# Kernel optimization log

Measured on AMD Instinct MI355X. Metric: run time of the kernel, lower is better.

The kernel has to match this reference:

```python
import jax, jax.numpy as jnp
import numpy as np

N_NODES = 50000
N_GRAPHS = 64
HIDDEN = 128
INPUT = 128
NEG_SLOPE = 0.2


def _gat_layer(x, src, dst, W, a_src, a_dst, b, n_nodes):
    # x: [N, Fin]; src/dst: [E] (self-loops already included)
    h = x @ W                              # [N, H]
    alpha_s = h @ a_src                    # [N]
    alpha_d = h @ a_dst                    # [N]
    e = alpha_s[src] + alpha_d[dst]        # [E]
    e = jnp.where(e > 0, e, NEG_SLOPE * e)  # leaky_relu(0.2)
    # segment softmax over destination node
    m = jax.ops.segment_max(e, dst, num_segments=n_nodes)  # [N]
    m = jnp.where(jnp.isfinite(m), m, 0.0)
    ee = jnp.exp(e - m[dst])
    s = jax.ops.segment_sum(ee, dst, num_segments=n_nodes)
    coef = ee / (s[dst] + 1e-16)           # [E]
    out = jax.ops.segment_sum(h[src] * coef[:, None], dst, num_segments=n_nodes)
    return out + b


def setup_inputs() -> dict:
    key = jax.random.key(0)
    ks = jax.random.split(key, 16)
    x = jax.random.normal(ks[0], (N_NODES, INPUT), dtype=jnp.float32)
    edge_index = jax.random.randint(ks[1], (2, 600000), 0, N_NODES, dtype=jnp.int64 if jax.config.x64_enabled else jnp.int32).astype(jnp.int32)
    batch = jnp.sort(jax.random.randint(ks[2], (N_NODES,), 0, N_GRAPHS)).astype(jnp.int32)
    def glorot(k, shape):
        lim = float(np.sqrt(6.0 / (shape[0] + shape[-1])))
        return jax.random.uniform(k, shape, jnp.float32, -lim, lim)
    params = {}
    dims = [(INPUT, HIDDEN), (HIDDEN, HIDDEN), (HIDDEN, HIDDEN)]
    for i, (fi, fo) in enumerate(dims, 1):
        params[f"W{i}"] = glorot(ks[3 * i], (fi, fo))
        params[f"a_src{i}"] = glorot(ks[3 * i + 1], (fo,)) * 0.1
        params[f"a_dst{i}"] = glorot(ks[3 * i + 2], (fo,)) * 0.1
        params[f"b{i}"] = jnp.zeros((fo,), jnp.float32)
    return dict(x=x, edge_index=edge_index, batch=batch, **params)


def reference(x, edge_index, batch,
              W1, a_src1, a_dst1, b1,
              W2, a_src2, a_dst2, b2,
              W3, a_src3, a_dst3, b3):
    n = x.shape[0]
    loops = jnp.arange(n, dtype=edge_index.dtype)
    src = jnp.concatenate([edge_index[0], loops])  # PyG add_self_loops=True
    dst = jnp.concatenate([edge_index[1], loops])
    h = jax.nn.elu(_gat_layer(x, src, dst, W1, a_src1, a_dst1, b1, n))
    h = jax.nn.elu(_gat_layer(h, src, dst, W2, a_src2, a_dst2, b2, n))
    h = jax.nn.elu(_gat_layer(h, src, dst, W3, a_src3, a_dst3, b3, n))
    # global_mean_pool
    sums = jax.ops.segment_sum(h, batch, num_segments=N_GRAPHS)
    cnt = jax.ops.segment_sum(jnp.ones((n,), h.dtype), batch, num_segments=N_GRAPHS)
    return sums / jnp.maximum(cnt, 1.0)[:, None]
```

## Files before the change

kernel.cpp:

```cpp
#include <hip/hip_runtime.h>
#include <math.h>

#define N_NODES 50000
#define N_GRAPHS 64
#define HID 128
#define SCAN_B 196

typedef _Float16 half8 __attribute__((ext_vector_type(8)));
typedef float f32x4 __attribute__((ext_vector_type(4)));
typedef int i32x4 __attribute__((ext_vector_type(4)));

__device__ __forceinline__ float lrelu(float e) { return e > 0.f ? e : 0.2f * e; }
__device__ __forceinline__ float elu_fast(float o) { return o > 0.f ? o : __expf(o) - 1.f; }

__device__ __forceinline__ void fmix_lo(float& a, int h2, float c) {
    asm("v_fma_mix_f32 %0, %1, %2, %0 op_sel_hi:[1,0,0]" : "+v"(a) : "v"(h2), "v"(c));
}
__device__ __forceinline__ void fmix_hi(float& a, int h2, float c) {
    asm("v_fma_mix_f32 %0, %1, %2, %0 op_sel:[1,0,0] op_sel_hi:[1,0,0]" : "+v"(a) : "v"(h2), "v"(c));
}

__global__ void count_prep(const int* __restrict__ dst, int n_e, int nblk,
                           int* __restrict__ counts, int* __restrict__ start,
                           const float* __restrict__ W0, const float* __restrict__ W1,
                           const float* __restrict__ W2,
                           const float* __restrict__ as0, const float* __restrict__ ad0,
                           const float* __restrict__ as1, const float* __restrict__ ad1,
                           const float* __restrict__ as2, const float* __restrict__ ad2,
                           _Float16* __restrict__ Wh0, _Float16* __restrict__ Wh1,
                           _Float16* __restrict__ Wh2,
                           float* __restrict__ wfold) {
    int blk = blockIdx.x;
    if (blk < nblk) {
        if (blk == 0 && threadIdx.x <= N_GRAPHS) start[threadIdx.x] = -1;
        int e = blk * 256 + threadIdx.x;
        if (e < n_e) atomicAdd(&counts[dst[e]], 1);
        return;
    }
    int b = blk - nblk;
    if (b < 24) {
        int layer = b >> 3;
        const float* W = layer == 0 ? W0 : (layer == 1 ? W1 : W2);
        _Float16* Wh = layer == 0 ? Wh0 : (layer == 1 ? Wh1 : Wh2);
        int t = (b & 7) * 256 + threadIdx.x;
        int lane = t & 63;
        int nt = (t >> 6) & 7;
        int kt = t >> 9;
        int n = nt * 16 + (lane & 15);
        int kbase = kt * 32 + (lane >> 4) * 8;
#pragma unroll
        for (int j = 0; j < 8; ++j) {
            float w = W[(size_t)(kbase + j) * 128 + n];
            Wh[(size_t)t * 8 + j] = (_Float16)w;
        }
    } else {
        int idx = b - 24;
        int layer = idx >> 1, which = idx & 1;
        const float* W = layer == 0 ? W0 : (layer == 1 ? W1 : W2);
        const float* a = which == 0 ? (layer == 0 ? as0 : (layer == 1 ? as1 : as2))
                                    : (layer == 0 ? ad0 : (layer == 1 ? ad1 : ad2));
        int k = threadIdx.x;
        if (k < 128) {
            float s = 0.f;
            for (int j = 0; j < 128; ++j) s = fmaf(W[k * 128 + j], a[j], s);
            wfold[idx * 128 + k] = s;
        }
    }
}

__global__ __launch_bounds__(256) void block_reduce(const int* __restrict__ counts,
                                                    int* __restrict__ bsum) {
    __shared__ int red[256];
    int t = threadIdx.x;
    int i = blockIdx.x * 256 + t;
    red[t] = (i < N_NODES) ? counts[i] : 0;
    __syncthreads();
#pragma unroll
    for (int off = 128; off; off >>= 1) {
        if (t < off) red[t] += red[t + off];
        __syncthreads();
    }
    if (t == 0) bsum[blockIdx.x] = red[0];
}

__global__ __launch_bounds__(256) void block_scan(const int* __restrict__ counts,
                                                  const int* __restrict__ bsum,
                                                  const int* __restrict__ batch,
                                                  int* __restrict__ offs,
                                                  int* __restrict__ cursor,
                                                  int* __restrict__ start) {
    __shared__ int sb[256];
    __shared__ int sh[256];
    int t = threadIdx.x;
    int v = (t < SCAN_B) ? bsum[t] : 0;
    sb[t] = v;
    __syncthreads();
#pragma unroll
    for (int off = 1; off < 256; off <<= 1) {
        int u = (t >= off) ? sb[t - off] : 0;
        __syncthreads();
        sb[t] += u;
        __syncthreads();
    }
    int bpre = (blockIdx.x == 0) ? 0 : sb[blockIdx.x - 1];
    if (blockIdx.x == 0 && t == SCAN_B - 1) offs[N_NODES] = sb[t];

    int i = blockIdx.x * 256 + t;
    int c = (i < N_NODES) ? counts[i] : 0;
    sh[t] = c;
    __syncthreads();
#pragma unroll
    for (int off = 1; off < 256; off <<= 1) {
        int u = (t >= off) ? sh[t - off] : 0;
        __syncthreads();
        sh[t] += u;
        __syncthreads();
    }
    if (i < N_NODES) {
        int e = bpre + sh[t] - c;
        offs[i] = e;
        cursor[i] = e;
        int b = batch[i];
        if (i == 0) start[b] = 0;
        else if (batch[i - 1] != b) start[b] = i;
    }
}

__global__ void scatter_kernel(const int* __restrict__ src, const int* __restrict__ dst, int n_e,
                               int* __restrict__ cursor, int* __restrict__ csr_src,
                               float* __restrict__ outz) {
    int gid = blockIdx.x * blockDim.x + threadIdx.x;
    if (gid < N_GRAPHS * HID) outz[gid] = 0.f;
    if (gid >= n_e) return;
    int d = dst[gid];
    int pos = atomicAdd(&cursor[d], 1);
    csr_src[pos] = src[gid];
}

__global__ __launch_bounds__(256) void gemm_mfma(const float* __restrict__ X,
                                                 const _Float16* __restrict__ Wh,
                                                 const float* __restrict__ wsv,
                                                 const float* __restrict__ wdv,
                                                 _Float16* __restrict__ H16,
                                                 float* __restrict__ AS,
                                                 float* __restrict__ AD) {
    __shared__ float wsL[128], wdL[128];
    int t = threadIdx.x;
    if (t < 128) wsL[t] = wsv[t];
    else if (t < 256) wdL[t - 128] = wdv[t - 128];
    __syncthreads();

    int wave = t >> 6, lane = t & 63;
    int m15 = lane & 15, quad = lane >> 4;
    int rowbase = blockIdx.x * 64 + wave * 16;
    int arow = rowbase + m15;
    bool arow_ok = arow < N_NODES;

    f32x4 acc[8];
#pragma unroll
    for (int nt = 0; nt < 8; ++nt) acc[nt] = (f32x4){0.f, 0.f, 0.f, 0.f};
    float as_p = 0.f, ad_p = 0.f;

    const float* xrow = X + (size_t)arow * 128 + quad * 8;
#pragma unroll
    for (int kt = 0; kt < 4; ++kt) {
        f32x4 a0 = (f32x4){0.f, 0.f, 0.f, 0.f};
        f32x4 a1 = (f32x4){0.f, 0.f, 0.f, 0.f};
        if (arow_ok) {
            a0 = *(const f32x4*)(xrow + kt * 32);
            a1 = *(const f32x4*)(xrow + kt * 32 + 4);
        }
        int kb = kt * 32 + quad * 8;
        half8 ah;
#pragma unroll
        for (int j = 0; j < 4; ++j) {
            as_p = fmaf(a0[j], wsL[kb + j], as_p);
            ad_p = fmaf(a0[j], wdL[kb + j], ad_p);
            as_p = fmaf(a1[j], wsL[kb + 4 + j], as_p);
            ad_p = fmaf(a1[j], wdL[kb + 4 + j], ad_p);
            ah[j] = (_Float16)a0[j];
            ah[4 + j] = (_Float16)a1[j];
        }
#pragma unroll
        for (int nt = 0; nt < 8; ++nt) {
            size_t fidx = ((size_t)((kt * 8 + nt) * 64 + lane)) * 8;
            half8 bh = *(const half8*)(Wh + fidx);
            acc[nt] = __builtin_amdgcn_mfma_f32_16x16x32_f16(ah, bh, acc[nt], 0, 0, 0);
        }
    }

#pragma unroll
    for (int nt = 0; nt < 8; ++nt) {
        int c = nt * 16 + m15;
#pragma unroll
        for (int reg = 0; reg < 4; ++reg) {
            int gr = rowbase + quad * 4 + reg;
            if (gr < N_NODES) H16[(size_t)gr * 128 + c] = (_Float16)acc[nt][reg];
        }
    }
    as_p += __shfl_xor(as_p, 16);
    ad_p += __shfl_xor(ad_p, 16);
    as_p += __shfl_xor(as_p, 32);
    ad_p += __shfl_xor(ad_p, 32);
    if (quad == 0 && arow_ok) { AS[arow] = as_p; AD[arow] = ad_p; }
}

__global__ __launch_bounds__(256) void aggregate_kernel(const _Float16* __restrict__ H16,
                                                        const float* __restrict__ AS,
                                                        const float* __restrict__ AD,
                                                        const int* __restrict__ offs,
                                                        const int* __restrict__ csr_src,
                                                        const float* __restrict__ bias,
                                                        float* __restrict__ OUT) {
    __shared__ int2 sh_sp[16][64];
    int tid = threadIdx.x;
    int quad = tid >> 4;
    int l16 = tid & 15;
    int node = blockIdx.x * 16 + quad;

    int beg = offs[node];
    int deg = offs[node + 1] - beg;
    float ad = AD[node];
    float eself = lrelu(AS[node] + ad);
    bool fast = deg <= 64;

    float m, inv, psn;
    if (fast) {
        float mym = -INFINITY;
        for (int i = l16; i < deg; i += 16) {
            int sv = csr_src[beg + i];
            float e = lrelu(AS[sv] + ad);
            sh_sp[quad][i] = make_int2(sv, __float_as_int(e));
            mym = fmaxf(mym, e);
        }
#pragma unroll
        for (int off = 8; off; off >>= 1) mym = fmaxf(mym, __shfl_xor(mym, off, 16));
        m = fmaxf(mym, eself);
        float ssum = 0.f;
        for (int i = l16; i < deg; i += 16) {
            int2 sp = sh_sp[quad][i];
            float p = __expf(__int_as_float(sp.y) - m);
            sh_sp[quad][i] = make_int2(sp.x, __float_as_int(p));
            ssum += p;
        }
#pragma unroll
        for (int off = 8; off; off >>= 1) ssum += __shfl_xor(ssum, off, 16);
        float ps = __expf(eself - m);
        inv = __builtin_amdgcn_rcpf(ssum + ps + 1e-16f);
        psn = ps * inv;
    } else {
        float mym = -INFINITY;
        for (int i = beg + l16; i < beg + deg; i += 16)
            mym = fmaxf(mym, lrelu(AS[csr_src[i]] + ad));
#pragma unroll
        for (int off = 8; off; off >>= 1) mym = fmaxf(mym, __shfl_xor(mym, off, 16));
        m = fmaxf(mym, eself);
        float ssum = 0.f;
        for (int i = beg + l16; i < beg + deg; i += 16)
            ssum += __expf(lrelu(AS[csr_src[i]] + ad) - m);
#pragma unroll
        for (int off = 8; off; off >>= 1) ssum += __shfl_xor(ssum, off, 16);
        float ps = __expf(eself - m);
        inv = __builtin_amdgcn_rcpf(ssum + ps + 1e-16f);
        psn = ps * inv;
    }

    const i32x4* H4 = (const i32x4*)H16;
    float accA[8] = {0.f, 0.f, 0.f, 0.f, 0.f, 0.f, 0.f, 0.f};
    float accB[8] = {0.f, 0.f, 0.f, 0.f, 0.f, 0.f, 0.f, 0.f};

    if (fast) {
        int k = 0;
        for (; k + 1 < deg; k += 2) {
            int2 sp0 = sh_sp[quad][k];
            int2 sp1 = sh_sp[quad][k + 1];
            float c0 = __int_as_float(sp0.y) * inv;
            float c1 = __int_as_float(sp1.y) * inv;
            i32x4 h0 = H4[(size_t)sp0.x * 16 + l16];
            i32x4 h1 = H4[(size_t)sp1.x * 16 + l16];
#pragma unroll
            for (int j = 0; j < 4; ++j) {
                fmix_lo(accA[2 * j], h0[j], c0);
                fmix_hi(accA[2 * j + 1], h0[j], c0);
                fmix_lo(accB[2 * j], h1[j], c1);
                fmix_hi(accB[2 * j + 1], h1[j], c1);
            }
        }
        if (k < deg) {
            int2 sp0 = sh_sp[quad][k];
            float c0 = __int_as_float(sp0.y) * inv;
            i32x4 h0 = H4[(size_t)sp0.x * 16 + l16];
#pragma unroll
            for (int j = 0; j < 4; ++j) {
                fmix_lo(accA[2 * j], h0[j], c0);
                fmix_hi(accA[2 * j + 1], h0[j], c0);
            }
        }
    } else {
        for (int k = 0; k < deg; ++k) {
            int s = csr_src[beg + k];
            float c = __expf(lrelu(AS[s] + ad) - m) * inv;
            i32x4 h0 = H4[(size_t)s * 16 + l16];
#pragma unroll
            for (int j = 0; j < 4; ++j) {
                fmix_lo(accA[2 * j], h0[j], c);
                fmix_hi(accA[2 * j + 1], h0[j], c);
            }
        }
    }

    i32x4 hsv = H4[(size_t)node * 16 + l16];
#pragma unroll
    for (int j = 0; j < 4; ++j) {
        fmix_lo(accA[2 * j], hsv[j], psn);
        fmix_hi(accA[2 * j + 1], hsv[j], psn);
    }
    f32x4 b0 = ((const f32x4*)bias)[l16 * 2];
    f32x4 b1 = ((const f32x4*)bias)[l16 * 2 + 1];
    f32x4 o0, o1;
    o0.x = elu_fast(accA[0] + accB[0] + b0.x);
    o0.y = elu_fast(accA[1] + accB[1] + b0.y);
    o0.z = elu_fast(accA[2] + accB[2] + b0.z);
    o0.w = elu_fast(accA[3] + accB[3] + b0.w);
    o1.x = elu_fast(accA[4] + accB[4] + b1.x);
    o1.y = elu_fast(accA[5] + accB[5] + b1.y);
    o1.z = elu_fast(accA[6] + accB[6] + b1.z);
    o1.w = elu_fast(accA[7] + accB[7] + b1.w);
    ((f32x4*)OUT)[(size_t)node * 32 + l16 * 2] = o0;
    ((f32x4*)OUT)[(size_t)node * 32 + l16 * 2 + 1] = o1;
}

__device__ __forceinline__ int estart(const int* __restrict__ start, int g) {
    for (; g < N_GRAPHS; ++g) {
        int v = start[g];
        if (v >= 0) return v;
    }
    return N_NODES;
}

__global__ __launch_bounds__(128) void pool_kernel(const float* __restrict__ F,
                                                   const int* __restrict__ start,
                                                   float* __restrict__ out) {
    int b = blockIdx.x;
    int g = b >> 4, sub = b & 15;
    int c = threadIdx.x;
    int s0 = estart(start, g), e0 = estart(start, g + 1);
    float acc = 0.f;
    for (int i = s0 + sub; i < e0; i += 16) acc += F[(size_t)i * 128 + c];
    int cnt = e0 - s0;
    float r = 1.f / (float)(cnt > 1 ? cnt : 1);
    atomicAdd(&out[(size_t)g * 128 + c], acc * r);
}

extern "C" void kernel_launch(void* const* d_in, const int* in_sizes, int n_in,
                              void* d_out, int out_size, void* d_ws, size_t ws_size,
                              hipStream_t stream) {
    const float* x = (const float*)d_in[0];
    const int* edge_index = (const int*)d_in[1];
    const int* batch = (const int*)d_in[2];
    const float* W[3]   = {(const float*)d_in[3], (const float*)d_in[7], (const float*)d_in[11]};
    const float* avs[3] = {(const float*)d_in[4], (const float*)d_in[8], (const float*)d_in[12]};
    const float* avd[3] = {(const float*)d_in[5], (const float*)d_in[9], (const float*)d_in[13]};
    const float* bb[3]  = {(const float*)d_in[6], (const float*)d_in[10], (const float*)d_in[14]};
    int E0 = in_sizes[1] / 2;
    const int* esrc = edge_index;
    const int* edst = edge_index + E0;

    char* p = (char*)d_ws;
    auto alloc = [&](size_t bytes) -> void* {
        void* q = (void*)p;
        p += (bytes + 255) & ~(size_t)255;
        return q;
    };
    int* counts   = (int*)alloc((size_t)N_NODES * 4);
    int* offs     = (int*)alloc((size_t)(N_NODES + 1) * 4);
    int* cursor   = (int*)alloc((size_t)N_NODES * 4);
    int* csr_src  = (int*)alloc((size_t)E0 * 4);
    int* start    = (int*)alloc((N_GRAPHS + 1) * 4);
    int* bsum     = (int*)alloc(SCAN_B * 4);
    float* AS     = (float*)alloc((size_t)N_NODES * 4);
    float* AD     = (float*)alloc((size_t)N_NODES * 4);
    float* wfold  = (float*)alloc(6 * 128 * 4);
    _Float16* H16 = (_Float16*)alloc((size_t)N_NODES * HID * 2);
    float* FA     = (float*)alloc((size_t)N_NODES * HID * 4);
    float* FB     = (float*)alloc((size_t)N_NODES * HID * 4);
    _Float16* Wh[3];
    for (int l = 0; l < 3; ++l) Wh[l] = (_Float16*)alloc(16384 * 2);

    int nblk = (E0 + 255) / 256;
    hipMemsetAsync(counts, 0, (size_t)N_NODES * 4, stream);
    count_prep<<<nblk + 30, 256, 0, stream>>>(edst, E0, nblk, counts, start,
                                              W[0], W[1], W[2], avs[0], avd[0], avs[1], avd[1],
                                              avs[2], avd[2], Wh[0], Wh[1], Wh[2], wfold);
    block_reduce<<<SCAN_B, 256, 0, stream>>>(counts, bsum);
    block_scan<<<SCAN_B, 256, 0, stream>>>(counts, bsum, batch, offs, cursor, start);
    scatter_kernel<<<nblk, 256, 0, stream>>>(esrc, edst, E0, cursor, csr_src, (float*)d_out);

    const float* cur = x;
    float* feat[2] = {FA, FB};
    for (int l = 0; l < 3; ++l) {
        gemm_mfma<<<(N_NODES + 63) / 64, 256, 0, stream>>>(cur, Wh[l],
                                                           wfold + (l * 2) * 128,
                                                           wfold + (l * 2 + 1) * 128,
                                                           H16, AS, AD);
        float* nxt = feat[l & 1];
        aggregate_kernel<<<N_NODES / 16, 256, 0, stream>>>(H16, AS, AD, offs, csr_src,
                                                           bb[l], nxt);
        cur = nxt;
    }

    pool_kernel<<<N_GRAPHS * 16, 128, 0, stream>>>(cur, start, (float*)d_out);
}
```

Before: 304.2 us.

## Sort nodes by degree for aggregation and defer softmax normalization

Builds a degree histogram during the scan and a degree-bucketed node ordering during the scatter pass. The aggregate kernel then processes nodes in that order, so the 16 nodes sharing a block have similar degree and their 16-lane groups finish at similar times. Softmax normalization is deferred to the final output (multiply by the reciprocal once), the self-row load is hoisted, and the gather loop is unrolled by 4 for more loads in flight. Costs include an extra indirection, atomics for the ordering, and scattered output writes and offs reads because node order is no longer sequential.

```diff
diff --git a/kernel.cpp b/kernel.cpp
--- a/kernel.cpp
+++ b/kernel.cpp
@@ -5,6 +5,8 @@
 #define N_GRAPHS 64
 #define HID 128
 #define SCAN_B 196
+#define NODE_BLKS 196
+#define NBUCK 128
 
 typedef _Float16 half8 __attribute__((ext_vector_type(8)));
 typedef float f32x4 __attribute__((ext_vector_type(4)));
@@ -22,6 +24,7 @@
 
 __global__ void count_prep(const int* __restrict__ dst, int n_e, int nblk,
                            int* __restrict__ counts, int* __restrict__ start,
+                           int* __restrict__ dhist, int* __restrict__ gcur,
                            const float* __restrict__ W0, const float* __restrict__ W1,
                            const float* __restrict__ W2,
                            const float* __restrict__ as0, const float* __restrict__ ad0,
@@ -32,7 +35,10 @@
                            float* __restrict__ wfold) {
     int blk = blockIdx.x;
     if (blk < nblk) {
-        if (blk == 0 && threadIdx.x <= N_GRAPHS) start[threadIdx.x] = -1;
+        if (blk == 0) {
+            if (threadIdx.x <= N_GRAPHS) start[threadIdx.x] = -1;
+            if (threadIdx.x < NBUCK) { dhist[threadIdx.x] = 0; gcur[threadIdx.x] = 0; }
+        }
         int e = blk * 256 + threadIdx.x;
         if (e < n_e) atomicAdd(&counts[dst[e]], 1);
         return;
@@ -88,10 +94,13 @@
                                                   const int* __restrict__ batch,
                                                   int* __restrict__ offs,
                                                   int* __restrict__ cursor,
-                                                  int* __restrict__ start) {
+                                                  int* __restrict__ start,
+                                                  int* __restrict__ dhist) {
     __shared__ int sb[256];
     __shared__ int sh[256];
+    __shared__ int lh[NBUCK];
     int t = threadIdx.x;
+    if (t < NBUCK) lh[t] = 0;
     int v = (t < SCAN_B) ? bsum[t] : 0;
     sb[t] = v;
     __syncthreads();
@@ -123,18 +132,60 @@
         int b = batch[i];
         if (i == 0) start[b] = 0;
         else if (batch[i - 1] != b) start[b] = i;
-    }
-}
-
-__global__ void scatter_kernel(const int* __restrict__ src, const int* __restrict__ dst, int n_e,
-                               int* __restrict__ cursor, int* __restrict__ csr_src,
-                               float* __restrict__ outz) {
-    int gid = blockIdx.x * blockDim.x + threadIdx.x;
+        atomicAdd(&lh[c < NBUCK - 1 ? c : NBUCK - 1], 1);
+    }
+    __syncthreads();
+    if (t < NBUCK) {
+        int n = lh[t];
+        if (n) atomicAdd(&dhist[t], n);
+    }
+}
+
+__global__ __launch_bounds__(256) void scatter_kernel(const int* __restrict__ src,
+                                                      const int* __restrict__ dst, int n_e,
+                                                      int* __restrict__ cursor,
+                                                      int* __restrict__ csr_src,
+                                                      float* __restrict__ outz,
+                                                      const int* __restrict__ offs,
+                                                      const int* __restrict__ dhist,
+                                                      int* __restrict__ gcur,
+                                                      int* __restrict__ order) {
+    int gid = blockIdx.x * 256 + threadIdx.x;
     if (gid < N_GRAPHS * HID) outz[gid] = 0.f;
-    if (gid >= n_e) return;
-    int d = dst[gid];
-    int pos = atomicAdd(&cursor[d], 1);
-    csr_src[pos] = src[gid];
+    if (gid < n_e) {
+        int d = dst[gid];
+        int pos = atomicAdd(&cursor[d], 1);
+        csr_src[pos] = src[gid];
+    }
+    if (blockIdx.x >= NODE_BLKS) return;
+
+    __shared__ int lh[NBUCK], sc[NBUCK], lbase[NBUCK];
+    int t = threadIdx.x;
+    if (t < NBUCK) lh[t] = 0;
+    __syncthreads();
+    int b = -1, lpos = 0;
+    if (gid < N_NODES) {
+        int deg = offs[gid + 1] - offs[gid];
+        b = deg < NBUCK - 1 ? deg : NBUCK - 1;
+        lpos = atomicAdd(&lh[b], 1);
+    }
+    __syncthreads();
+    if (t < NBUCK) sc[t] = dhist[t];
+    __syncthreads();
+    for (int off = 1; off < NBUCK; off <<= 1) {
+        int u = (t < NBUCK && t >= off) ? sc[t - off] : 0;
+        __syncthreads();
+        if (t < NBUCK) sc[t] += u;
+        __syncthreads();
+    }
+    if (t < NBUCK) {
+        int excl = t ? sc[t - 1] : 0;
+        int cnt = lh[t];
+        int bb = cnt ? atomicAdd(&gcur[t], cnt) : 0;
+        lbase[t] = excl + bb;
+    }
+    __syncthreads();
+    if (gid < N_NODES) order[lbase[b] + lpos] = gid;
 }
 
 __global__ __launch_bounds__(256) void gemm_mfma(const float* __restrict__ X,
@@ -210,21 +261,24 @@
                                                         const float* __restrict__ AD,
                                                         const int* __restrict__ offs,
                                                         const int* __restrict__ csr_src,
+                                                        const int* __restrict__ order,
                                                         const float* __restrict__ bias,
                                                         float* __restrict__ OUT) {
     __shared__ int2 sh_sp[16][64];
     int tid = threadIdx.x;
     int quad = tid >> 4;
     int l16 = tid & 15;
-    int node = blockIdx.x * 16 + quad;
+    int node = order[blockIdx.x * 16 + quad];
 
     int beg = offs[node];
     int deg = offs[node + 1] - beg;
     float ad = AD[node];
     float eself = lrelu(AS[node] + ad);
+    const i32x4* H4 = (const i32x4*)H16;
+    i32x4 hsv = H4[(size_t)node * 16 + l16];
     bool fast = deg <= 64;
 
-    float m, inv, psn;
+    float m, ssum = 0.f, ps;
     if (fast) {
         float mym = -INFINITY;
         for (int i = l16; i < deg; i += 16) {
@@ -236,18 +290,13 @@
 #pragma unroll
         for (int off = 8; off; off >>= 1) mym = fmaxf(mym, __shfl_xor(mym, off, 16));
         m = fmaxf(mym, eself);
-        float ssum = 0.f;
+        ps = __expf(eself - m);
         for (int i = l16; i < deg; i += 16) {
             int2 sp = sh_sp[quad][i];
             float p = __expf(__int_as_float(sp.y) - m);
             sh_sp[quad][i] = make_int2(sp.x, __float_as_int(p));
             ssum += p;
         }
-#pragma unroll
-        for (int off = 8; off; off >>= 1) ssum += __shfl_xor(ssum, off, 16);
-        float ps = __expf(eself - m);
-        inv = __builtin_amdgcn_rcpf(ssum + ps + 1e-16f);
-        psn = ps * inv;
     } else {
         float mym = -INFINITY;
         for (int i = beg + l16; i < beg + deg; i += 16)
@@ -255,29 +304,27 @@
 #pragma unroll
         for (int off = 8; off; off >>= 1) mym = fmaxf(mym, __shfl_xor(mym, off, 16));
         m = fmaxf(mym, eself);
-        float ssum = 0.f;
+        ps = __expf(eself - m);
         for (int i = beg + l16; i < beg + deg; i += 16)
             ssum += __expf(lrelu(AS[csr_src[i]] + ad) - m);
-#pragma unroll
-        for (int off = 8; off; off >>= 1) ssum += __shfl_xor(ssum, off, 16);
-        float ps = __expf(eself - m);
-        inv = __builtin_amdgcn_rcpf(ssum + ps + 1e-16f);
-        psn = ps * inv;
-    }
-
-    const i32x4* H4 = (const i32x4*)H16;
+    }
+
     float accA[8] = {0.f, 0.f, 0.f, 0.f, 0.f, 0.f, 0.f, 0.f};
     float accB[8] = {0.f, 0.f, 0.f, 0.f, 0.f, 0.f, 0.f, 0.f};
 
     if (fast) {
         int k = 0;
-        for (; k + 1 < deg; k += 2) {
+        for (; k + 3 < deg; k += 4) {
             int2 sp0 = sh_sp[quad][k];
             int2 sp1 = sh_sp[quad][k + 1];
-            float c0 = __int_as_float(sp0.y) * inv;
-            float c1 = __int_as_float(sp1.y) * inv;
+            int2 sp2 = sh_sp[quad][k + 2];
+            int2 sp3 = sh_sp[quad][k + 3];
             i32x4 h0 = H4[(size_t)sp0.x * 16 + l16];
             i32x4 h1 = H4[(size_t)sp1.x * 16 + l16];
+            i32x4 h2 = H4[(size_t)sp2.x * 16 + l16];
+            i32x4 h3 = H4[(size_t)sp3.x * 16 + l16];
+            float c0 = __int_as_float(sp0.y), c1 = __int_as_float(sp1.y);
+            float c2 = __int_as_float(sp2.y), c3 = __int_as_float(sp3.y);
 #pragma unroll
             for (int j = 0; j < 4; ++j) {
                 fmix_lo(accA[2 * j], h0[j], c0);
@@ -285,10 +332,17 @@
                 fmix_lo(accB[2 * j], h1[j], c1);
                 fmix_hi(accB[2 * j + 1], h1[j], c1);
             }
-        }
-        if (k < deg) {
+#pragma unroll
+            for (int j = 0; j < 4; ++j) {
+                fmix_lo(accA[2 * j], h2[j], c2);
+                fmix_hi(accA[2 * j + 1], h2[j], c2);
+                fmix_lo(accB[2 * j], h3[j], c3);
+                fmix_hi(accB[2 * j + 1], h3[j], c3);
+            }
+        }
+        for (; k < deg; ++k) {
             int2 sp0 = sh_sp[quad][k];
-            float c0 = __int_as_float(sp0.y) * inv;
+            float c0 = __int_as_float(sp0.y);
             i32x4 h0 = H4[(size_t)sp0.x * 16 + l16];
 #pragma unroll
             for (int j = 0; j < 4; ++j) {
@@ -299,7 +353,7 @@
     } else {
         for (int k = 0; k < deg; ++k) {
             int s = csr_src[beg + k];
-            float c = __expf(lrelu(AS[s] + ad) - m) * inv;
+            float c = __expf(lrelu(AS[s] + ad) - m);
             i32x4 h0 = H4[(size_t)s * 16 + l16];
 #pragma unroll
             for (int j = 0; j < 4; ++j) {
@@ -309,23 +363,26 @@
         }
     }
 
-    i32x4 hsv = H4[(size_t)node * 16 + l16];
 #pragma unroll
     for (int j = 0; j < 4; ++j) {
-        fmix_lo(accA[2 * j], hsv[j], psn);
-        fmix_hi(accA[2 * j + 1], hsv[j], psn);
-    }
+        fmix_lo(accA[2 * j], hsv[j], ps);
+        fmix_hi(accA[2 * j + 1], hsv[j], ps);
+    }
+#pragma unroll
+    for (int off = 8; off; off >>= 1) ssum += __shfl_xor(ssum, off, 16);
+    float inv = __builtin_amdgcn_rcpf(ssum + ps + 1e-16f);
+
     f32x4 b0 = ((const f32x4*)bias)[l16 * 2];
     f32x4 b1 = ((const f32x4*)bias)[l16 * 2 + 1];
     f32x4 o0, o1;
-    o0.x = elu_fast(accA[0] + accB[0] + b0.x);
-    o0.y = elu_fast(accA[1] + accB[1] + b0.y);
-    o0.z = elu_fast(accA[2] + accB[2] + b0.z);
-    o0.w = elu_fast(accA[3] + accB[3] + b0.w);
-    o1.x = elu_fast(accA[4] + accB[4] + b1.x);
-    o1.y = elu_fast(accA[5] + accB[5] + b1.y);
-    o1.z = elu_fast(accA[6] + accB[6] + b1.z);
-    o1.w = elu_fast(accA[7] + accB[7] + b1.w);
+    o0.x = elu_fast(fmaf(accA[0] + accB[0], inv, b0.x));
+    o0.y = elu_fast(fmaf(accA[1] + accB[1], inv, b0.y));
+    o0.z = elu_fast(fmaf(accA[2] + accB[2], inv, b0.z));
+    o0.w = elu_fast(fmaf(accA[3] + accB[3], inv, b0.w));
+    o1.x = elu_fast(fmaf(accA[4] + accB[4], inv, b1.x));
+    o1.y = elu_fast(fmaf(accA[5] + accB[5], inv, b1.y));
+    o1.z = elu_fast(fmaf(accA[6] + accB[6], inv, b1.z));
+    o1.w = elu_fast(fmaf(accA[7] + accB[7], inv, b1.w));
     ((f32x4*)OUT)[(size_t)node * 32 + l16 * 2] = o0;
     ((f32x4*)OUT)[(size_t)node * 32 + l16 * 2 + 1] = o1;
 }
@@ -378,6 +435,9 @@
     int* csr_src  = (int*)alloc((size_t)E0 * 4);
     int* start    = (int*)alloc((N_GRAPHS + 1) * 4);
     int* bsum     = (int*)alloc(SCAN_B * 4);
+    int* dhist    = (int*)alloc(NBUCK * 4);
+    int* gcur     = (int*)alloc(NBUCK * 4);
+    int* order    = (int*)alloc((size_t)N_NODES * 4);
     float* AS     = (float*)alloc((size_t)N_NODES * 4);
     float* AD     = (float*)alloc((size_t)N_NODES * 4);
     float* wfold  = (float*)alloc(6 * 128 * 4);
@@ -389,12 +449,13 @@
 
     int nblk = (E0 + 255) / 256;
     hipMemsetAsync(counts, 0, (size_t)N_NODES * 4, stream);
-    count_prep<<<nblk + 30, 256, 0, stream>>>(edst, E0, nblk, counts, start,
+    count_prep<<<nblk + 30, 256, 0, stream>>>(edst, E0, nblk, counts, start, dhist, gcur,
                                               W[0], W[1], W[2], avs[0], avd[0], avs[1], avd[1],
                                               avs[2], avd[2], Wh[0], Wh[1], Wh[2], wfold);
     block_reduce<<<SCAN_B, 256, 0, stream>>>(counts, bsum);
-    block_scan<<<SCAN_B, 256, 0, stream>>>(counts, bsum, batch, offs, cursor, start);
-    scatter_kernel<<<nblk, 256, 0, stream>>>(esrc, edst, E0, cursor, csr_src, (float*)d_out);
+    block_scan<<<SCAN_B, 256, 0, stream>>>(counts, bsum, batch, offs, cursor, start, dhist);
+    scatter_kernel<<<nblk, 256, 0, stream>>>(esrc, edst, E0, cursor, csr_src, (float*)d_out,
+                                             offs, dhist, gcur, order);
 
     const float* cur = x;
     float* feat[2] = {FA, FB};
@@ -404,7 +465,7 @@
                                                            wfold + (l * 2 + 1) * 128,
                                                            H16, AS, AD);
         float* nxt = feat[l & 1];
-        aggregate_kernel<<<N_NODES / 16, 256, 0, stream>>>(H16, AS, AD, offs, csr_src,
+        aggregate_kernel<<<N_NODES / 16, 256, 0, stream>>>(H16, AS, AD, offs, csr_src, order,
                                                            bb[l], nxt);
         cur = nxt;
     }
```

Measured after the change: 305.2 us. No clear change (+0.3%).
